# Kernel tuning notes

Hardware: AMD Instinct MI355X
Metric: run time of the kernel (lower is better)

## Reference

```python
import jax, jax.numpy as jnp
import numpy as np

B, N, HD = 2, 2048, 2048
NH, KVH = 16, 4
D = HD // NH          # 128
R = NH // KVH         # 4 (kv_ratio)
KVD = KVH * D         # 512


def setup_inputs() -> dict:
    key = jax.random.key(0)
    ks = jax.random.split(key, 6)
    s = 0.02
    return {
        "tokens": jax.random.normal(ks[0], (B, N, HD), jnp.float32),
        "norm_w": jnp.ones((HD,), jnp.float32),
        "Wq": jax.random.normal(ks[1], (HD, HD), jnp.float32) * s,
        "bq": jnp.zeros((HD,), jnp.float32),
        "Wk": jax.random.normal(ks[2], (KVD, HD), jnp.float32) * s,
        "bk": jnp.zeros((KVD,), jnp.float32),
        "Wv": jax.random.normal(ks[3], (KVD, HD), jnp.float32) * s,
        "bv": jnp.zeros((KVD,), jnp.float32),
        "Wo": jax.random.normal(ks[4], (HD, HD), jnp.float32) * s,
        "bo": jnp.zeros((HD,), jnp.float32),
    }


def reference(tokens, norm_w, Wq, bq, Wk, bk, Wv, bv, Wo, bo):
    # RMSNorm (torch default eps=None -> finfo eps), learnable weight
    eps = jnp.finfo(tokens.dtype).eps
    x = tokens * jax.lax.rsqrt(jnp.mean(tokens * tokens, axis=-1, keepdims=True) + eps) * norm_w

    # projections -> [B, heads, N, D]
    q = (x @ Wq.T + bq).reshape(B, N, NH, D).transpose(0, 2, 1, 3)
    k = (x @ Wk.T + bk).reshape(B, N, KVH, D).transpose(0, 2, 1, 3)
    v = (x @ Wv.T + bv).reshape(B, N, KVH, D).transpose(0, 2, 1, 3)

    # GQA via tiling the kv block (matches torch.cat of copies: head h uses kv head h % KVH)
    k = jnp.tile(k, (1, R, 1, 1))
    v = jnp.tile(v, (1, R, 1, 1))

    # Faithful (inverted) mask: True where j <= i, and True positions are masked out.
    mask = jnp.arange(N)[None, :] <= jnp.arange(N)[:, None]  # [N, N]

    # No 1/sqrt(D) scaling in the original
    scores = jnp.einsum('bhid,bhjd->bhij', q, k)
    scores = jnp.where(mask[None, None, :, :], jnp.float32(-1e9), scores)
    attn = jax.nn.softmax(scores, axis=-1)

    a = jnp.einsum('bhij,bhjd->bhid', attn, v)       # [B, NH, N, D]
    a = a.transpose(0, 2, 1, 3).reshape(B, N, HD)    # [B, N, HD]
    return a @ Wo.T + bo
```

## Files before the change

### kernel.cpp

```cpp
#include <hip/hip_runtime.h>

#define BB   2
#define NN   2048
#define HDIM 2048
#define NHD  16
#define KVHD 4
#define DD   128
#define KVW  1024
#define MTOK (BB*NN)
#define NSPLIT 7

typedef _Float16 h8 __attribute__((ext_vector_type(8)));
typedef _Float16 h4 __attribute__((ext_vector_type(4)));
typedef float    f4 __attribute__((ext_vector_type(4)));
typedef float    fx16 __attribute__((ext_vector_type(16)));
typedef short    b8 __attribute__((ext_vector_type(8)));
typedef unsigned int u4v __attribute__((ext_vector_type(4)));

static __device__ __forceinline__ fx16 mfma32h(h8 a, h8 b, fx16 c) {
    return __builtin_amdgcn_mfma_f32_32x32x16_f16(a, b, c, 0, 0, 0);
}
static __device__ __forceinline__ f4 mfma16(h8 a, h8 b, f4 c) {
    return __builtin_amdgcn_mfma_f32_16x16x32_f16(a, b, c, 0, 0, 0);
}
static __device__ __forceinline__ fx16 mfma32b(b8 a, b8 b, fx16 c) {
    return __builtin_amdgcn_mfma_f32_32x32x16_bf16(a, b, c, 0, 0, 0);
}

static __device__ __forceinline__ unsigned short f2bf(float f) {
    unsigned int u = __float_as_uint(f);
    u += 0x7FFF + ((u >> 16) & 1);
    return (unsigned short)(u >> 16);
}

static __device__ __forceinline__ void gload_lds16(const void* g, void* l) {
    __builtin_amdgcn_global_load_lds(
        (const __attribute__((address_space(1))) void*)g,
        (__attribute__((address_space(3))) void*)l, 16, 0, 0);
}

__global__ __launch_bounds__(256) void rmsnorm_k(const float* __restrict__ t,
                                                 const float* __restrict__ wn,
                                                 _Float16* __restrict__ xh) {
    const int row = blockIdx.x, tid = threadIdx.x;
    const float* rp = t + (size_t)row * HDIM;
    float4 v[2];
    float ss = 0.f;
    #pragma unroll
    for (int p = 0; p < 2; ++p) {
        float4 x = *(const float4*)(rp + (p * 256 + tid) * 4);
        v[p] = x;
        ss += x.x * x.x + x.y * x.y + x.z * x.z + x.w * x.w;
    }
    #pragma unroll
    for (int off = 32; off; off >>= 1) ss += __shfl_xor(ss, off, 64);
    __shared__ float sred[4];
    if ((tid & 63) == 0) sred[tid >> 6] = ss;
    __syncthreads();
    float rs = rsqrtf((sred[0] + sred[1] + sred[2] + sred[3]) * (1.0f / HDIM)
                      + 1.1920928955078125e-07f);
    _Float16* op = xh + (size_t)row * HDIM;
    #pragma unroll
    for (int p = 0; p < 2; ++p) {
        int base = (p * 256 + tid) * 4;
        float4 w = *(const float4*)(wn + base);
        h4 o;
        o[0] = (_Float16)(v[p].x * rs * w.x);
        o[1] = (_Float16)(v[p].y * rs * w.y);
        o[2] = (_Float16)(v[p].z * rs * w.z);
        o[3] = (_Float16)(v[p].w * rs * w.w);
        *(h4*)(op + base) = o;
    }
}

__global__ __launch_bounds__(256) void cvtall_k(const float* __restrict__ Wq,
                                                const float* __restrict__ Wk,
                                                const float* __restrict__ Wv,
                                                const float* __restrict__ Wo,
                                                _Float16* __restrict__ wq_h,
                                                _Float16* __restrict__ wkv_h,
                                                _Float16* __restrict__ wo_h) {
    int blk = blockIdx.x;
    const float* src; _Float16* dst; int off;
    if (blk < 4096)      { src = Wq; dst = wq_h;               off = blk; }
    else if (blk < 5120) { src = Wk; dst = wkv_h;              off = blk - 4096; }
    else if (blk < 6144) { src = Wv; dst = wkv_h + 512 * HDIM; off = blk - 5120; }
    else                 { src = Wo; dst = wo_h;               off = blk - 6144; }
    int i = off * 1024 + threadIdx.x * 4;
    float4 v = *(const float4*)(src + i);
    h4 o; o[0] = (_Float16)v.x; o[1] = (_Float16)v.y;
    o[2] = (_Float16)v.z; o[3] = (_Float16)v.w;
    *(h4*)(dst + i) = o;
}

__global__ void biascat_k(const float* __restrict__ bq, const float* __restrict__ bk,
                          const float* __restrict__ bv,
                          float* __restrict__ bqkv, float* __restrict__ vsum) {
    int i = blockIdx.x * 256 + threadIdx.x;
    bqkv[i] = (i < 2048) ? bq[i] : (i < 2560) ? bk[i - 2048] : bv[i - 2560];
    if (i < 1024) vsum[i] = 0.f;
}

__global__ __launch_bounds__(256) void vtrans_k(const _Float16* __restrict__ kv,
                                                unsigned short* __restrict__ vt) {
    const int tid = threadIdx.x;
    const int tok = blockIdx.x * 64 + (tid & 63);
    const int kvh = blockIdx.y;
    const int d0 = (tid >> 6) * 32;
    const int b = tok >> 11, n = tok & (NN - 1);
    const int n2 = (n & ~12) | ((n & 4) << 1) | ((n & 8) >> 1);
    const _Float16* src = kv + (size_t)tok * KVW + 512 + kvh * DD + d0;
    unsigned short* dstb = vt + ((size_t)(b * KVHD + kvh) * DD) * NN + n2;
    #pragma unroll
    for (int u = 0; u < 4; ++u) {
        h8 v = *(const h8*)(src + u * 8);
        #pragma unroll
        for (int e = 0; e < 8; ++e)
            dstb[(size_t)(d0 + u * 8 + e) * NN] = f2bf((float)v[e]);
    }
}

template <int MODE>
__global__ __launch_bounds__(256, 2) void gemm_bt(const _Float16* __restrict__ A,
                                                  const _Float16* __restrict__ Bw,
                                                  const float* __restrict__ bias,
                                                  void* __restrict__ Cout,
                                                  void* __restrict__ Cout2,
                                                  int Ndim, int K) {
    __shared__ _Float16 sA[128 * 64];
    __shared__ _Float16 sB[128 * 64];
    const int tid = threadIdx.x;
    const int lane = tid & 63, w = tid >> 6;
    const int ln = lane & 15, quad = lane >> 4;
    const int wm = w >> 1, wn = w & 1;
    const int m0 = blockIdx.y * 128, n0 = blockIdx.x * 128;

    f4 acc[4][4] = {};
    for (int k0 = 0; k0 < K; k0 += 64) {
        #pragma unroll
        for (int it = 0; it < 4; ++it) {
            int chunk = it * 256 + tid;
            int row = chunk >> 3, p = chunk & 7;
            int c = p ^ (row & 7);
            gload_lds16(A + (size_t)(m0 + row) * K + k0 + c * 8, sA + chunk * 8);
            gload_lds16(Bw + (size_t)(n0 + row) * K + k0 + c * 8, sB + chunk * 8);
        }
        __syncthreads();
        #pragma unroll
        for (int kk = 0; kk < 2; ++kk) {
            h8 af[4], bf[4];
            #pragma unroll
            for (int mt = 0; mt < 4; ++mt)
                af[mt] = *(const h8*)&sA[(wm * 64 + mt * 16 + ln) * 64 +
                                         (((kk * 4 + quad) ^ (ln & 7)) << 3)];
            #pragma unroll
            for (int nt = 0; nt < 4; ++nt)
                bf[nt] = *(const h8*)&sB[(wn * 64 + nt * 16 + ln) * 64 +
                                         (((kk * 4 + quad) ^ (ln & 7)) << 3)];
            #pragma unroll
            for (int mt = 0; mt < 4; ++mt)
                #pragma unroll
                for (int nt = 0; nt < 4; ++nt)
                    acc[mt][nt] = mfma16(af[mt], bf[nt], acc[mt][nt]);
        }
        __syncthreads();
    }
    #pragma unroll
    for (int mt = 0; mt < 4; ++mt) {
        int rowb = m0 + wm * 64 + mt * 16 + quad * 4;
        #pragma unroll
        for (int nt = 0; nt < 4; ++nt) {
            int col = n0 + wn * 64 + nt * 16 + ln;
            float bv = bias[col];
            #pragma unroll
            for (int r = 0; r < 4; ++r) {
                float v = acc[mt][nt][r] + bv;
                if (MODE == 1)
                    ((float*)Cout)[(size_t)(rowb + r) * Ndim + col] = v;
                else {
                    if (n0 < 2048)
                        ((_Float16*)Cout)[(size_t)(rowb + r) * HDIM + col] = (_Float16)v;
                    else
                        ((_Float16*)Cout2)[(size_t)(rowb + r) * KVW + (col - 2048)] = (_Float16)v;
                }
            }
        }
    }
}

__device__ __constant__ int piece_tab[23] = {
    7,
    0x10000, 0x10100,
    8,
    0x10001, 0x10101,
    0x10002, 0x10102,
    9,
    0x10003, 0x10103,
    0x10004, 0x10104,
    10,
    0x10005, 0x10105,
    0x10006, 0x10106,
    11, 12, 13, 14, 15
};

__global__ __launch_bounds__(256, 2) void attn_k(const _Float16* __restrict__ qh,
                                                 const _Float16* __restrict__ kvp,
                                                 const unsigned short* __restrict__ vt,
                                                 _Float16* __restrict__ ah,
                                                 float* __restrict__ O_ws,
                                                 float* __restrict__ l_ws) {
    __shared__ _Float16 s_k[2][64 * 128];
    __shared__ unsigned short s_v[2][128 * 64];
    const int tid = threadIdx.x;
    const int lane = tid & 63, w = tid >> 6;
    const int l5 = lane & 31, hi = lane >> 5;
    const int idx = blockIdx.x;
    const int hb = idx & 31;
    const int h = hb & 15, b = hb >> 4;
    const int code = piece_tab[idx >> 5];
    const int x = code & 255, p = (code >> 8) & 1;
    const bool is_split = (code >> 16) & 1;
    int jlo, jhi;
    if (is_split) { int len = 16 - x; jlo = 2 * x + p * len; jhi = jlo + len; }
    else          { jlo = 2 * x; jhi = 32; }
    const int i0 = x * 128;
    const int kvh = h & 3;
    const int qg = i0 + w * 32 + l5;

    h8 qf[8];
    {
        const _Float16* qrow =
            qh + ((size_t)(b * NN + qg)) * HDIM + h * DD;
        #pragma unroll
        for (int kc = 0; kc < 8; ++kc)
            qf[kc] = *(const h8*)(qrow + kc * 16 + hi * 8);
    }

    b8 ones;
    #pragma unroll
    for (int e = 0; e < 8; ++e) ones[e] = (short)0x3F80;

    fx16 O[4] = {};
    fx16 OS = {};

    auto stage = [&](int jt, int bufi) {
        const int j0s = jt * 64;
        #pragma unroll
        for (int itr = 0; itr < 4; ++itr) {
            int chunk = itr * 256 + tid;
            int jj = chunk >> 4, pp = chunk & 15;
            int c = pp ^ (jj & 15) ^ ((jj >> 3) & 3);
            gload_lds16(kvp + ((size_t)(b * NN + j0s + jj)) * KVW + kvh * DD + c * 8,
                        &s_k[bufi][chunk * 8]);
        }
        #pragma unroll
        for (int itr = 0; itr < 4; ++itr) {
            int chunk = itr * 256 + tid;
            int d = chunk >> 3, pp = chunk & 7;
            int c = pp ^ (d & 7) ^ ((d >> 3) & 3);
            gload_lds16(vt + ((size_t)(b * KVHD + kvh) * DD + d) * NN + j0s + c * 8,
                        &s_v[bufi][chunk * 8]);
        }
    };

    stage(jlo, 0);
    for (int jt = jlo; jt < jhi; ++jt) {
        const int j0 = jt * 64;
        const int cur = (jt - jlo) & 1;
        __syncthreads();
        if (jt + 1 < jhi) stage(jt + 1, cur ^ 1);

        fx16 sc0 = {}, sc1 = {};
        #pragma unroll
        for (int kc = 0; kc < 8; ++kc) {
            int cs = ((kc * 2 + hi) ^ (l5 & 15) ^ ((l5 >> 3) & 3)) << 3;
            h8 k0 = *(const h8*)&s_k[cur][l5 * 128 + cs];
            h8 k1 = *(const h8*)&s_k[cur][(32 + l5) * 128 + cs];
            sc0 = mfma32h(k0, qf[kc], sc0);
            sc1 = mfma32h(k1, qf[kc], sc1);
        }

        const bool need_mask = (jt < 2 * x + 2);
        #pragma unroll
        for (int jb = 0; jb < 2; ++jb) {
            const fx16& sc = jb ? sc1 : sc0;
            unsigned int pwod[8];
            #pragma unroll
            for (int pr = 0; pr < 8; ++pr) {
                float s0 = sc[2 * pr], s1 = sc[2 * pr + 1];
                if (need_mask) {
                    int rg0 = 2 * pr;
                    int jg0 = j0 + jb * 32 + (rg0 & 3) + 8 * (rg0 >> 2) + 4 * hi;
                    if (jg0 <= qg) s0 = -1e9f;
                    if (jg0 + 1 <= qg) s1 = -1e9f;
                }
                pwod[pr] = (unsigned int)f2bf(__expf(s0)) |
                           ((unsigned int)f2bf(__expf(s1)) << 16);
            }
            u4v w0v = {pwod[0], pwod[1], pwod[2], pwod[3]};
            u4v w1v = {pwod[4], pwod[5], pwod[6], pwod[7]};
            b8 pa0 = __builtin_bit_cast(b8, w0v);
            b8 pa1 = __builtin_bit_cast(b8, w1v);

            #pragma unroll
            for (int ks = 0; ks < 2; ++ks) {
                b8 pa = ks ? pa1 : pa0;
                #pragma unroll
                for (int dblk = 0; dblk < 4; ++dblk) {
                    b8 bv = *(const b8*)&s_v[cur][(dblk * 32 + l5) * 64 +
                             (((jb * 4 + ks * 2 + hi) ^ (l5 & 7) ^ ((l5 >> 3) & 3)) << 3)];
                    O[dblk] = mfma32b(pa, bv, O[dblk]);
                }
                OS = mfma32b(pa, ones, OS);
            }
        }
    }

    if (is_split) {
        size_t po = (((size_t)(b * NHD + h) * NSPLIT + x) * 2 + p);
        float* Op = O_ws + po * 16384;
        float* Lp = l_ws + po * 128;
        #pragma unroll
        for (int nt4 = 0; nt4 < 4; ++nt4)
            #pragma unroll
            for (int rg = 0; rg < 16; ++rg) {
                int q = (rg & 3) + 8 * (rg >> 2) + 4 * hi;
                Op[(w * 32 + q) * 128 + nt4 * 32 + l5] = O[nt4][rg];
            }
        if (l5 == 0) {
            #pragma unroll
            for (int rg = 0; rg < 16; ++rg) {
                int q = (rg & 3) + 8 * (rg >> 2) + 4 * hi;
                Lp[w * 32 + q] = OS[rg];
            }
        }
    } else {
        float inv_l[16];
        #pragma unroll
        for (int rg = 0; rg < 16; ++rg) inv_l[rg] = 1.0f / OS[rg];
        #pragma unroll
        for (int nt4 = 0; nt4 < 4; ++nt4)
            #pragma unroll
            for (int rg = 0; rg < 16; ++rg) {
                int q = (rg & 3) + 8 * (rg >> 2) + 4 * hi;
                ah[((size_t)(b * NN + i0 + w * 32 + q)) * HDIM + h * DD + nt4 * 32 + l5] =
                    (_Float16)(O[nt4][rg] * inv_l[rg]);
            }
    }
}

__global__ __launch_bounds__(256) void combine_k(const float* __restrict__ O_ws,
                                                 const float* __restrict__ l_ws,
                                                 _Float16* __restrict__ ah) {
    const int x = blockIdx.x, h = blockIdx.y, b = blockIdx.z;
    const int tid = threadIdx.x;
    const int d = tid & 127;
    size_t po = (((size_t)(b * NHD + h) * NSPLIT + x) * 2);
    const float* O0 = O_ws + po * 16384;
    const float* O1 = O0 + 16384;
    const float* L0 = l_ws + po * 128;
    const float* L1 = L0 + 128;
    for (int ql = tid >> 7; ql < 128; ql += 2) {
        float l = L0[ql] + L1[ql];
        float o = O0[ql * 128 + d] + O1[ql * 128 + d];
        ah[((size_t)(b * NN + x * 128 + ql)) * HDIM + h * DD + d] = (_Float16)(o / l);
    }
}

__global__ __launch_bounds__(256) void vsum_k(const _Float16* __restrict__ kvp,
                                              float* __restrict__ vsum) {
    __shared__ float red[16][128];
    const int seg = blockIdx.x, kvh = blockIdx.y, b = blockIdx.z;
    const int tid = threadIdx.x;
    const int jj = tid >> 4, dc = (tid & 15) * 8;
    float acc[8] = {};
    #pragma unroll 4
    for (int j = seg * 256 + jj; j < seg * 256 + 256; j += 16) {
        h8 v = *(const h8*)(kvp + ((size_t)(b * NN + j)) * KVW + 512 + kvh * DD + dc);
        #pragma unroll
        for (int e = 0; e < 8; ++e) acc[e] += (float)v[e];
    }
    #pragma unroll
    for (int e = 0; e < 8; ++e) red[jj][dc + e] = acc[e];
    __syncthreads();
    if (tid < 128) {
        float s = 0.f;
        #pragma unroll
        for (int t = 0; t < 16; ++t) s += red[t][tid];
        atomicAdd(&vsum[(b * KVHD + kvh) * DD + tid], s);
    }
}

__global__ void fixup_write_k(const float* __restrict__ vsum,
                              _Float16* __restrict__ ah) {
    int b = blockIdx.x >> 2, kvh = blockIdx.x & 3, d = threadIdx.x;
    float mean = vsum[(b * KVHD + kvh) * DD + d] * (1.0f / NN);
    #pragma unroll
    for (int r = 0; r < 4; ++r) {
        int h = r * 4 + kvh;
        ah[((size_t)(b * NN + NN - 1)) * HDIM + h * DD + d] = (_Float16)mean;
    }
}

extern "C" void kernel_launch(void* const* d_in, const int* in_sizes, int n_in,
                              void* d_out, int out_size, void* d_ws, size_t ws_size,
                              hipStream_t stream) {
    const float* tokens = (const float*)d_in[0];
    const float* norm_w = (const float*)d_in[1];
    const float* Wq = (const float*)d_in[2];
    const float* bq = (const float*)d_in[3];
    const float* Wk = (const float*)d_in[4];
    const float* bk = (const float*)d_in[5];
    const float* Wv = (const float*)d_in[6];
    const float* bv = (const float*)d_in[7];
    const float* Wo = (const float*)d_in[8];
    const float* bo = (const float*)d_in[9];
    float* out = (float*)d_out;

    char* ws = (char*)d_ws;
    _Float16* x_h   = (_Float16*)(ws);
    _Float16* wq_h  = (_Float16*)(ws + 16777216);
    _Float16* wkv_h = (_Float16*)(ws + 25165824);
    _Float16* wo_h  = (_Float16*)(ws + 29360128);
    _Float16* q_h   = (_Float16*)(ws + 37752832);
    _Float16* kv_h  = (_Float16*)(ws + 54530048);
    _Float16* a_h   = (_Float16*)(ws + 62918656);
    unsigned short* vt_h = (unsigned short*)(ws + 79695872);
    float*    vsum  = (float*)   (ws + 83890176);
    float*    l_ws  = (float*)   (ws + 83894272);
    float*    bqkv  = (float*)   (ws + 84123648);
    float*    O_ws  = (float*)(ws);

    rmsnorm_k<<<MTOK, 256, 0, stream>>>(tokens, norm_w, x_h);
    cvtall_k<<<10240, 256, 0, stream>>>(Wq, Wk, Wv, Wo, wq_h, wkv_h, wo_h);
    biascat_k<<<12, 256, 0, stream>>>(bq, bk, bv, bqkv, vsum);

    gemm_bt<2><<<dim3(3072 / 128, MTOK / 128), 256, 0, stream>>>(
        x_h, wq_h, bqkv, (void*)q_h, (void*)kv_h, 3072, HDIM);

    vtrans_k<<<dim3(MTOK / 64, KVHD), 256, 0, stream>>>(kv_h, vt_h);

    attn_k<<<736, 256, 0, stream>>>(q_h, kv_h, vt_h, a_h, O_ws, l_ws);
    combine_k<<<dim3(NSPLIT, NHD, BB), 256, 0, stream>>>(O_ws, l_ws, a_h);
    vsum_k<<<dim3(8, KVHD, BB), 256, 0, stream>>>(kv_h, vsum);
    fixup_write_k<<<BB * KVHD, 128, 0, stream>>>(vsum, a_h);

    gemm_bt<1><<<dim3(HDIM / 128, MTOK / 128), 256, 0, stream>>>(
        a_h, wo_h, bo, (void*)out, nullptr, HDIM, HDIM);
}
```

Before: 316.4 us.

## Fuse prep kernels, move V transpose and V-sum into QKV GEMM epilogue

Merges the RMSNorm, weight-conversion and bias-concatenation kernels into one launch. The V transpose to bf16 and the per-head V column sums now happen in the epilogue of the QKV GEMM, so those blocks no longer write V to the kv buffer and the separate vtrans and vsum passes are gone. The fully-masked last-row fixup becomes an extra slice of the combine kernel. This removes several launches and a re-read of V, but the epilogue writes transposed V as scattered 2-byte stores and adds atomics, which may coalesce poorly.

```diff
diff --git a/kernel.cpp b/kernel.cpp
--- a/kernel.cpp
+++ b/kernel.cpp
@@ -39,85 +39,66 @@
         (__attribute__((address_space(3))) void*)l, 16, 0, 0);
 }
 
-__global__ __launch_bounds__(256) void rmsnorm_k(const float* __restrict__ t,
-                                                 const float* __restrict__ wn,
-                                                 _Float16* __restrict__ xh) {
-    const int row = blockIdx.x, tid = threadIdx.x;
-    const float* rp = t + (size_t)row * HDIM;
-    float4 v[2];
-    float ss = 0.f;
-    #pragma unroll
-    for (int p = 0; p < 2; ++p) {
-        float4 x = *(const float4*)(rp + (p * 256 + tid) * 4);
-        v[p] = x;
-        ss += x.x * x.x + x.y * x.y + x.z * x.z + x.w * x.w;
-    }
-    #pragma unroll
-    for (int off = 32; off; off >>= 1) ss += __shfl_xor(ss, off, 64);
-    __shared__ float sred[4];
-    if ((tid & 63) == 0) sred[tid >> 6] = ss;
-    __syncthreads();
-    float rs = rsqrtf((sred[0] + sred[1] + sred[2] + sred[3]) * (1.0f / HDIM)
-                      + 1.1920928955078125e-07f);
-    _Float16* op = xh + (size_t)row * HDIM;
-    #pragma unroll
-    for (int p = 0; p < 2; ++p) {
-        int base = (p * 256 + tid) * 4;
-        float4 w = *(const float4*)(wn + base);
-        h4 o;
-        o[0] = (_Float16)(v[p].x * rs * w.x);
-        o[1] = (_Float16)(v[p].y * rs * w.y);
-        o[2] = (_Float16)(v[p].z * rs * w.z);
-        o[3] = (_Float16)(v[p].w * rs * w.w);
-        *(h4*)(op + base) = o;
-    }
-}
-
-__global__ __launch_bounds__(256) void cvtall_k(const float* __restrict__ Wq,
-                                                const float* __restrict__ Wk,
-                                                const float* __restrict__ Wv,
-                                                const float* __restrict__ Wo,
-                                                _Float16* __restrict__ wq_h,
-                                                _Float16* __restrict__ wkv_h,
-                                                _Float16* __restrict__ wo_h) {
+__global__ __launch_bounds__(256) void prep_k(
+    const float* __restrict__ tokens, const float* __restrict__ wn,
+    const float* __restrict__ Wq, const float* __restrict__ Wk,
+    const float* __restrict__ Wv, const float* __restrict__ Wo,
+    const float* __restrict__ bq, const float* __restrict__ bk,
+    const float* __restrict__ bv,
+    _Float16* __restrict__ xh, _Float16* __restrict__ wq_h,
+    _Float16* __restrict__ wkv_h, _Float16* __restrict__ wo_h,
+    float* __restrict__ bqkv, float* __restrict__ vsum) {
+    const int tid = threadIdx.x;
     int blk = blockIdx.x;
-    const float* src; _Float16* dst; int off;
-    if (blk < 4096)      { src = Wq; dst = wq_h;               off = blk; }
-    else if (blk < 5120) { src = Wk; dst = wkv_h;              off = blk - 4096; }
-    else if (blk < 6144) { src = Wv; dst = wkv_h + 512 * HDIM; off = blk - 5120; }
-    else                 { src = Wo; dst = wo_h;               off = blk - 6144; }
-    int i = off * 1024 + threadIdx.x * 4;
-    float4 v = *(const float4*)(src + i);
-    h4 o; o[0] = (_Float16)v.x; o[1] = (_Float16)v.y;
-    o[2] = (_Float16)v.z; o[3] = (_Float16)v.w;
-    *(h4*)(dst + i) = o;
-}
-
-__global__ void biascat_k(const float* __restrict__ bq, const float* __restrict__ bk,
-                          const float* __restrict__ bv,
-                          float* __restrict__ bqkv, float* __restrict__ vsum) {
-    int i = blockIdx.x * 256 + threadIdx.x;
+    if (blk < MTOK) {
+        __shared__ float sred[4];
+        const float* rp = tokens + (size_t)blk * HDIM;
+        float4 v[2];
+        float ss = 0.f;
+        #pragma unroll
+        for (int p = 0; p < 2; ++p) {
+            float4 x = *(const float4*)(rp + (p * 256 + tid) * 4);
+            v[p] = x;
+            ss += x.x * x.x + x.y * x.y + x.z * x.z + x.w * x.w;
+        }
+        #pragma unroll
+        for (int off = 32; off; off >>= 1) ss += __shfl_xor(ss, off, 64);
+        if ((tid & 63) == 0) sred[tid >> 6] = ss;
+        __syncthreads();
+        float rs = rsqrtf((sred[0] + sred[1] + sred[2] + sred[3]) * (1.0f / HDIM)
+                          + 1.1920928955078125e-07f);
+        _Float16* op = xh + (size_t)blk * HDIM;
+        #pragma unroll
+        for (int p = 0; p < 2; ++p) {
+            int base = (p * 256 + tid) * 4;
+            float4 w = *(const float4*)(wn + base);
+            h4 o;
+            o[0] = (_Float16)(v[p].x * rs * w.x);
+            o[1] = (_Float16)(v[p].y * rs * w.y);
+            o[2] = (_Float16)(v[p].z * rs * w.z);
+            o[3] = (_Float16)(v[p].w * rs * w.w);
+            *(h4*)(op + base) = o;
+        }
+        return;
+    }
+    blk -= MTOK;
+    if (blk < 10240) {
+        const float* src; _Float16* dst; int off;
+        if (blk < 4096)      { src = Wq; dst = wq_h;               off = blk; }
+        else if (blk < 5120) { src = Wk; dst = wkv_h;              off = blk - 4096; }
+        else if (blk < 6144) { src = Wv; dst = wkv_h + 512 * HDIM; off = blk - 5120; }
+        else                 { src = Wo; dst = wo_h;               off = blk - 6144; }
+        int i = off * 1024 + tid * 4;
+        float4 v = *(const float4*)(src + i);
+        h4 o; o[0] = (_Float16)v.x; o[1] = (_Float16)v.y;
+        o[2] = (_Float16)v.z; o[3] = (_Float16)v.w;
+        *(h4*)(dst + i) = o;
+        return;
+    }
+    blk -= 10240;
+    int i = blk * 256 + tid;
     bqkv[i] = (i < 2048) ? bq[i] : (i < 2560) ? bk[i - 2048] : bv[i - 2560];
     if (i < 1024) vsum[i] = 0.f;
-}
-
-__global__ __launch_bounds__(256) void vtrans_k(const _Float16* __restrict__ kv,
-                                                unsigned short* __restrict__ vt) {
-    const int tid = threadIdx.x;
-    const int tok = blockIdx.x * 64 + (tid & 63);
-    const int kvh = blockIdx.y;
-    const int d0 = (tid >> 6) * 32;
-    const int b = tok >> 11, n = tok & (NN - 1);
-    const int n2 = (n & ~12) | ((n & 4) << 1) | ((n & 8) >> 1);
-    const _Float16* src = kv + (size_t)tok * KVW + 512 + kvh * DD + d0;
-    unsigned short* dstb = vt + ((size_t)(b * KVHD + kvh) * DD) * NN + n2;
-    #pragma unroll
-    for (int u = 0; u < 4; ++u) {
-        h8 v = *(const h8*)(src + u * 8);
-        #pragma unroll
-        for (int e = 0; e < 8; ++e)
-            dstb[(size_t)(d0 + u * 8 + e) * NN] = f2bf((float)v[e]);
-    }
 }
 
 template <int MODE>
@@ -126,6 +107,8 @@
                                                   const float* __restrict__ bias,
                                                   void* __restrict__ Cout,
                                                   void* __restrict__ Cout2,
+                                                  unsigned short* __restrict__ vt,
+                                                  float* __restrict__ vsum,
                                                   int Ndim, int K) {
     __shared__ _Float16 sA[128 * 64];
     __shared__ _Float16 sB[128 * 64];
@@ -165,6 +148,37 @@
         }
         __syncthreads();
     }
+
+    if (MODE == 2 && n0 >= 2560) {
+        #pragma unroll
+        for (int nt = 0; nt < 4; ++nt) {
+            int col = n0 + wn * 64 + nt * 16 + ln;
+            int vd = col - 2560, kvh = vd >> 7, d = vd & 127;
+            float bvb = bias[col];
+            float vs = 0.f;
+            #pragma unroll
+            for (int mt = 0; mt < 4; ++mt) {
+                int rowb = m0 + wm * 64 + mt * 16 + quad * 4;
+                #pragma unroll
+                for (int r = 0; r < 4; ++r) {
+                    _Float16 hv = (_Float16)(acc[mt][nt][r] + bvb);
+                    float fv = (float)hv;
+                    int token = rowb + r;
+                    int n = token & (NN - 1);
+                    int n2 = (n & ~12) | ((n & 4) << 1) | ((n & 8) >> 1);
+                    vt[((size_t)((token >> 11) * KVHD + kvh) * DD + d) * NN + n2] =
+                        f2bf(fv);
+                    vs += fv;
+                }
+            }
+            vs += __shfl_xor(vs, 16, 64);
+            vs += __shfl_xor(vs, 32, 64);
+            if (quad == 0)
+                atomicAdd(&vsum[((size_t)(m0 >> 11) * KVHD + kvh) * DD + d], vs);
+        }
+        return;
+    }
+
     #pragma unroll
     for (int mt = 0; mt < 4; ++mt) {
         int rowb = m0 + wm * 64 + mt * 16 + quad * 4;
@@ -351,9 +365,17 @@
 
 __global__ __launch_bounds__(256) void combine_k(const float* __restrict__ O_ws,
                                                  const float* __restrict__ l_ws,
+                                                 const float* __restrict__ vsum,
                                                  _Float16* __restrict__ ah) {
     const int x = blockIdx.x, h = blockIdx.y, b = blockIdx.z;
     const int tid = threadIdx.x;
+    if (x == NSPLIT) {
+        if (tid < 128) {
+            float mean = vsum[((size_t)b * KVHD + (h & 3)) * DD + tid] * (1.0f / NN);
+            ah[((size_t)(b * NN + NN - 1)) * HDIM + h * DD + tid] = (_Float16)mean;
+        }
+        return;
+    }
     const int d = tid & 127;
     size_t po = (((size_t)(b * NHD + h) * NSPLIT + x) * 2);
     const float* O0 = O_ws + po * 16384;
@@ -364,41 +386,6 @@
         float l = L0[ql] + L1[ql];
         float o = O0[ql * 128 + d] + O1[ql * 128 + d];
         ah[((size_t)(b * NN + x * 128 + ql)) * HDIM + h * DD + d] = (_Float16)(o / l);
-    }
-}
-
-__global__ __launch_bounds__(256) void vsum_k(const _Float16* __restrict__ kvp,
-                                              float* __restrict__ vsum) {
-    __shared__ float red[16][128];
-    const int seg = blockIdx.x, kvh = blockIdx.y, b = blockIdx.z;
-    const int tid = threadIdx.x;
-    const int jj = tid >> 4, dc = (tid & 15) * 8;
-    float acc[8] = {};
-    #pragma unroll 4
-    for (int j = seg * 256 + jj; j < seg * 256 + 256; j += 16) {
-        h8 v = *(const h8*)(kvp + ((size_t)(b * NN + j)) * KVW + 512 + kvh * DD + dc);
-        #pragma unroll
-        for (int e = 0; e < 8; ++e) acc[e] += (float)v[e];
-    }
-    #pragma unroll
-    for (int e = 0; e < 8; ++e) red[jj][dc + e] = acc[e];
-    __syncthreads();
-    if (tid < 128) {
-        float s = 0.f;
-        #pragma unroll
-        for (int t = 0; t < 16; ++t) s += red[t][tid];
-        atomicAdd(&vsum[(b * KVHD + kvh) * DD + tid], s);
-    }
-}
-
-__global__ void fixup_write_k(const float* __restrict__ vsum,
-                              _Float16* __restrict__ ah) {
-    int b = blockIdx.x >> 2, kvh = blockIdx.x & 3, d = threadIdx.x;
-    float mean = vsum[(b * KVHD + kvh) * DD + d] * (1.0f / NN);
-    #pragma unroll
-    for (int r = 0; r < 4; ++r) {
-        int h = r * 4 + kvh;
-        ah[((size_t)(b * NN + NN - 1)) * HDIM + h * DD + d] = (_Float16)mean;
     }
 }
 
@@ -431,20 +418,17 @@
     float*    bqkv  = (float*)   (ws + 84123648);
     float*    O_ws  = (float*)(ws);
 
-    rmsnorm_k<<<MTOK, 256, 0, stream>>>(tokens, norm_w, x_h);
-    cvtall_k<<<10240, 256, 0, stream>>>(Wq, Wk, Wv, Wo, wq_h, wkv_h, wo_h);
-    biascat_k<<<12, 256, 0, stream>>>(bq, bk, bv, bqkv, vsum);
+    prep_k<<<MTOK + 10240 + 12, 256, 0, stream>>>(
+        tokens, norm_w, Wq, Wk, Wv, Wo, bq, bk, bv,
+        x_h, wq_h, wkv_h, wo_h, bqkv, vsum);
 
     gemm_bt<2><<<dim3(3072 / 128, MTOK / 128), 256, 0, stream>>>(
-        x_h, wq_h, bqkv, (void*)q_h, (void*)kv_h, 3072, HDIM);
-
-    vtrans_k<<<dim3(MTOK / 64, KVHD), 256, 0, stream>>>(kv_h, vt_h);
+        x_h, wq_h, bqkv, (void*)q_h, (void*)kv_h, vt_h, vsum, 3072, HDIM);
 
     attn_k<<<736, 256, 0, stream>>>(q_h, kv_h, vt_h, a_h, O_ws, l_ws);
-    combine_k<<<dim3(NSPLIT, NHD, BB), 256, 0, stream>>>(O_ws, l_ws, a_h);
-    vsum_k<<<dim3(8, KVHD, BB), 256, 0, stream>>>(kv_h, vsum);
-    fixup_write_k<<<BB * KVHD, 128, 0, stream>>>(vsum, a_h);
+
+    combine_k<<<dim3(NSPLIT + 1, NHD, BB), 256, 0, stream>>>(O_ws, l_ws, vsum, a_h);
 
     gemm_bt<1><<<dim3(HDIM / 128, MTOK / 128), 256, 0, stream>>>(
-        a_h, wo_h, bo, (void*)out, nullptr, HDIM, HDIM);
-}
+        a_h, wo_h, bo, (void*)out, nullptr, nullptr, nullptr, HDIM, HDIM);
+}
```

After: 299.4 us. -5.4%, faster.
